# Performance work log

Measured on AMD Instinct MI355X. Metric: run time of the kernel, lower is better.

The kernel has to match this reference:

```python
import jax, jax.numpy as jnp
import numpy as np

B, T, D_MODEL = 1, 4096, 1024
H = 16
SEM_DIM, GEO_DIM, ATTN_DIM = 128, 256, 512
SEM_HD, GEO_HD, V_HD = SEM_DIM // H, GEO_DIM // H, ATTN_DIM // H
ROPE_BASE = 10000.0


def _split_heads(x, hd):
    # (B,T,H*hd) -> (B,H,T,hd)
    b, t, _ = x.shape
    return x.reshape(b, t, H, hd).transpose(0, 2, 1, 3)


def _rope(x, pos_offset, base=ROPE_BASE):
    # x: (B,H,T,rot) with rot == full geo head dim (rotate applies to first rot_dim;
    # here rot_dim == geo_head_dim so the whole vector rotates)
    rot = x.shape[-1]
    inv_freq = 1.0 / (base ** (jnp.arange(0, rot, 2, dtype=jnp.float32) / rot))
    t = jnp.arange(pos_offset, pos_offset + x.shape[2], dtype=jnp.float32)
    freqs = t[:, None] * inv_freq[None, :]            # (T, rot/2)
    cos = jnp.cos(freqs).astype(x.dtype)[None, None]  # (1,1,T,rot/2)
    sin = jnp.sin(freqs).astype(x.dtype)[None, None]
    x1, x2 = x[..., : rot // 2], x[..., rot // 2 :]
    return jnp.concatenate([x1 * cos - x2 * sin, x1 * sin + x2 * cos], axis=-1)


def setup_inputs() -> dict:
    key = jax.random.key(0)
    ks = jax.random.split(key, 8)
    s = lambda fan_in: 1.0 / np.sqrt(fan_in)
    inp = {
        "x": jax.random.normal(ks[0], (B, T, D_MODEL), dtype=jnp.float32),
        "q_sem_w": jax.random.uniform(ks[1], (SEM_DIM, D_MODEL), jnp.float32, -s(D_MODEL), s(D_MODEL)),
        "k_sem_w": jax.random.uniform(ks[2], (SEM_DIM, D_MODEL), jnp.float32, -s(D_MODEL), s(D_MODEL)),
        "q_geo_w": jax.random.uniform(ks[3], (GEO_DIM, D_MODEL), jnp.float32, -s(D_MODEL), s(D_MODEL)),
        "k_geo_w": jax.random.uniform(ks[4], (GEO_DIM, D_MODEL), jnp.float32, -s(D_MODEL), s(D_MODEL)),
        "v_w": jax.random.uniform(ks[5], (ATTN_DIM, D_MODEL), jnp.float32, -s(D_MODEL), s(D_MODEL)),
        "out_w": jax.random.uniform(ks[6], (D_MODEL, ATTN_DIM), jnp.float32, -s(ATTN_DIM), s(ATTN_DIM)),
        "logit_scale": jnp.zeros((H,), dtype=jnp.float32),
        "attn_mask": jnp.tril(jnp.ones((T, T), dtype=bool)),  # causal: True = attend
        "pos_offset": 0,
    }
    return inp


def reference(x, q_sem_w, k_sem_w, q_geo_w, k_geo_w, v_w, out_w, logit_scale, attn_mask, pos_offset):
    dt = x.dtype
    ninf = jnp.finfo(dt).min
    # decoupled projections
    qs = _split_heads(x @ q_sem_w.T, SEM_HD)   # (B,H,T,sem_hd)
    ksem = _split_heads(x @ k_sem_w.T, SEM_HD)
    qg = _split_heads(x @ q_geo_w.T, GEO_HD)   # (B,H,T,geo_hd)
    kg = _split_heads(x @ k_geo_w.T, GEO_HD)
    v = _split_heads(x @ v_w.T, V_HD)          # (B,H,T,v_hd)
    # RoPE on geometric stream only
    qg = _rope(qg, pos_offset)
    kg = _rope(kg, pos_offset)
    # combined scores, scaled as one concatenated QK dot product
    scale = 1.0 / np.sqrt(SEM_HD + GEO_HD)
    scores = (jnp.einsum("bhtd,bhsd->bhts", qs, ksem)
              + jnp.einsum("bhtd,bhsd->bhts", qg, kg)) * scale
    # learned per-head temperature
    scores = scores * jnp.exp(logit_scale)[None, :, None, None]
    scores = jnp.where(attn_mask[None, None], scores, ninf)
    attn = jax.nn.softmax(scores, axis=-1)
    out = jnp.einsum("bhts,bhsd->bhtd", attn, v)       # (B,H,T,v_hd)
    out = out.transpose(0, 2, 1, 3).reshape(B, T, ATTN_DIM)
    return out @ out_w.T                                # (B,T,d_model)
```

## Files before the change

### kernel.cpp

```cpp
#include <hip/hip_runtime.h>
#include <hip/hip_bf16.h>

typedef __attribute__((ext_vector_type(8))) short short8;
typedef __attribute__((ext_vector_type(4))) short short4v;
typedef __attribute__((ext_vector_type(4))) float f32x4;

#define TT 4096
#define DM 1024
#define NH 16
#define NPROJ 1280
#define DATTN 512

static __device__ __forceinline__ short f2bf(float f) {
  __hip_bfloat16 h = __float2bfloat16(f);
  return *reinterpret_cast<short*>(&h);
}

#define NB_X   (TT * DM / 4 / 256)
#define NB_OW  (DM * DATTN / 4 / 256)
#define NB_WC  (NPROJ * DM / 4 / 256)
__global__ __launch_bounds__(256) void k_prep(const float* __restrict__ x,
    const float* __restrict__ ow, const float* __restrict__ qs, const float* __restrict__ ks,
    const float* __restrict__ qg, const float* __restrict__ kg, const float* __restrict__ vw,
    __hip_bfloat16* __restrict__ Xbf, __hip_bfloat16* __restrict__ OW,
    __hip_bfloat16* __restrict__ Wcat) {
  const int b = blockIdx.x;
  if (b < NB_X) {
    const int i = b * 256 + threadIdx.x;
    float4 v = reinterpret_cast<const float4*>(x)[i];
    short4v o;
    o[0] = f2bf(v.x); o[1] = f2bf(v.y); o[2] = f2bf(v.z); o[3] = f2bf(v.w);
    reinterpret_cast<short4v*>(Xbf)[i] = o;
  } else if (b < NB_X + NB_OW) {
    const int i = (b - NB_X) * 256 + threadIdx.x;
    float4 v = reinterpret_cast<const float4*>(ow)[i];
    short4v o;
    o[0] = f2bf(v.x); o[1] = f2bf(v.y); o[2] = f2bf(v.z); o[3] = f2bf(v.w);
    reinterpret_cast<short4v*>(OW)[i] = o;
  } else {
    const int i = (b - NB_X - NB_OW) * 256 + threadIdx.x;
    const int idx = i * 4;
    const int row = idx >> 10;
    const int col = idx & 1023;
    const float* src;
    if (row < 128)      src = qs + (size_t)row * DM;
    else if (row < 256) src = ks + (size_t)(row - 128) * DM;
    else if (row < 512) src = qg + (size_t)(row - 256) * DM;
    else if (row < 768) src = kg + (size_t)(row - 512) * DM;
    else                src = vw + (size_t)(row - 768) * DM;
    float4 v = *reinterpret_cast<const float4*>(src + col);
    short4v o;
    o[0] = f2bf(v.x); o[1] = f2bf(v.y); o[2] = f2bf(v.z); o[3] = f2bf(v.w);
    *reinterpret_cast<short4v*>(Wcat + idx) = o;
  }
}

template<int EPI>
__global__ __launch_bounds__(256) void k_gemm_bt(const __hip_bfloat16* __restrict__ A,
    const __hip_bfloat16* __restrict__ B, void* __restrict__ Cv, int M, int N, int K,
    __hip_bfloat16* __restrict__ Qp, __hip_bfloat16* __restrict__ Kp,
    __hip_bfloat16* __restrict__ Vt, const float* __restrict__ ls,
    const int* __restrict__ posp) {
  __shared__ alignas(16) __hip_bfloat16 lA[2][2][64 * 32];
  __shared__ alignas(16) __hip_bfloat16 lB[2][2][128 * 32];
  const int tid = threadIdx.x;
  const int lane = tid & 63;
  const int wid = tid >> 6;
  const int m0 = blockIdx.x * 64, n0 = blockIdx.y * 128;
  const int wm = (wid >> 1) * 32, wn = (wid & 1) * 64;
  const int srow = tid >> 2;
  const int scol = (tid & 3) * 8;
  const int fr = lane & 15, fk = (lane >> 4) * 8;
  f32x4 acc[2][4];
  const f32x4 zz = {0.f, 0.f, 0.f, 0.f};
#pragma unroll
  for (int m = 0; m < 2; ++m)
#pragma unroll
    for (int n = 0; n < 4; ++n) acc[m][n] = zz;

  auto stage = [&](int kt, int buf) {
#pragma unroll
    for (int kk = 0; kk < 2; ++kk) {
      const int kcol = kt + kk * 32 + scol;
      const __hip_bfloat16* ga0 = A + (size_t)(m0 + srow) * K + kcol;
      const __hip_bfloat16* gb0 = B + (size_t)(n0 + srow) * K + kcol;
      const __hip_bfloat16* gb1 = B + (size_t)(n0 + 64 + srow) * K + kcol;
      __builtin_amdgcn_global_load_lds((const __attribute__((address_space(1))) void*)ga0,
          (__attribute__((address_space(3))) void*)(lA[buf][kk] + srow * 32 + scol), 16, 0, 0);
      __builtin_amdgcn_global_load_lds((const __attribute__((address_space(1))) void*)gb0,
          (__attribute__((address_space(3))) void*)(lB[buf][kk] + srow * 32 + scol), 16, 0, 0);
      __builtin_amdgcn_global_load_lds((const __attribute__((address_space(1))) void*)gb1,
          (__attribute__((address_space(3))) void*)(lB[buf][kk] + (64 + srow) * 32 + scol), 16, 0, 0);
    }
  };
  stage(0, 0);
  int buf = 0;
  for (int kt = 0; kt < K; kt += 64) {
    __syncthreads();
    if (kt + 64 < K) stage(kt + 64, buf ^ 1);
#pragma unroll
    for (int kk = 0; kk < 2; ++kk) {
      short8 af[2], bfr[4];
#pragma unroll
      for (int m = 0; m < 2; ++m)
        af[m] = *reinterpret_cast<const short8*>(lA[buf][kk] + (wm + m * 16 + fr) * 32 + fk);
#pragma unroll
      for (int n = 0; n < 4; ++n)
        bfr[n] = *reinterpret_cast<const short8*>(lB[buf][kk] + (wn + n * 16 + fr) * 32 + fk);
#pragma unroll
      for (int m = 0; m < 2; ++m)
#pragma unroll
        for (int n = 0; n < 4; ++n)
          acc[m][n] = __builtin_amdgcn_mfma_f32_16x16x32_bf16(af[m], bfr[n], acc[m][n], 0, 0, 0);
    }
    buf ^= 1;
  }
  const int cr = (lane >> 4) * 4, cc = lane & 15;
  if (EPI == 0) {
#pragma unroll
    for (int m = 0; m < 2; ++m)
#pragma unroll
      for (int n = 0; n < 4; ++n)
#pragma unroll
        for (int j = 0; j < 4; ++j) {
          const int row = m0 + wm + m * 16 + cr + j;
          const int col = n0 + wn + n * 16 + cc;
          ((float*)Cv)[(size_t)row * N + col] = acc[m][n][j];
        }
    return;
  }
  const int y = blockIdx.y;
  const float QSC = 0.20412414523193154f * 1.4426950408889634f;
  if (y < 2) {
    __hip_bfloat16* P = (y == 0) ? Qp : Kp;
    const __hip_bfloat16 zb = __float2bfloat16(0.f);
#pragma unroll
    for (int n = 0; n < 4; ++n) {
      const int cl = wn + n * 16 + cc;
      const int h = cl >> 3, d = cl & 7;
      const float sc = (y == 0) ? QSC * __expf(ls[h]) : 1.0f;
#pragma unroll
      for (int m = 0; m < 2; ++m)
#pragma unroll
        for (int j = 0; j < 4; ++j) {
          const int row = m0 + wm + m * 16 + cr + j;
          __hip_bfloat16* base = P + ((size_t)h * TT + row) * 32;
          base[d] = __float2bfloat16(acc[m][n][j] * sc);
          base[24 + d] = zb;
        }
    }
  } else if (y < 6) {
    const int isQ = (y < 4);
    __hip_bfloat16* P = isQ ? Qp : Kp;
    const int segbase = isQ ? 256 : 512;
    const float invf[8] = {1.0f, 0.31622776601683794f, 0.1f, 0.031622776601683794f,
                           0.01f, 0.0031622776601683794f, 0.001f, 0.00031622776601683794f};
    const float fr_ = invf[cc & 7];
    const float pofs = (float)posp[0];
    const int lo = (cc < 8);
    const int d = 8 + cc;
#pragma unroll
    for (int n = 0; n < 4; ++n) {
      const int h = (y * 128 + wn + n * 16 - segbase) >> 4;
      const float sc = isQ ? QSC * __expf(ls[h]) : 1.0f;
#pragma unroll
      for (int m = 0; m < 2; ++m)
#pragma unroll
        for (int j = 0; j < 4; ++j) {
          const int row = m0 + wm + m * 16 + cr + j;
          const float own = acc[m][n][j];
          const float oth = __shfl_xor(own, 8, 64);
          float ss, cs;
          __sincosf((row + pofs) * fr_, &ss, &cs);
          const float out = lo ? (own * cs - oth * ss) : (oth * ss + own * cs);
          P[((size_t)h * TT + row) * 32 + d] = __float2bfloat16(out * sc);
        }
    }
  } else {
#pragma unroll
    for (int n = 0; n < 4; ++n) {
      const int local = y * 128 + wn + n * 16 - 768 + cc;
      const int h = local >> 5, d = local & 31;
#pragma unroll
      for (int m = 0; m < 2; ++m) {
        short4v pk;
#pragma unroll
        for (int j = 0; j < 4; ++j) pk[j] = f2bf(acc[m][n][j]);
        const int row0 = m0 + wm + m * 16 + cr;
        *reinterpret_cast<short4v*>(Vt + ((size_t)h * 32 + d) * TT + row0) = pk;
      }
    }
  }
}

__global__ __launch_bounds__(256) void k_attn(const __hip_bfloat16* __restrict__ Qp,
    const __hip_bfloat16* __restrict__ Kp, const __hip_bfloat16* __restrict__ Vt,
    __hip_bfloat16* __restrict__ Ob) {
  __shared__ alignas(16) __hip_bfloat16 lK[2][64 * 32];
  __shared__ alignas(16) __hip_bfloat16 lV[2][32 * 64];
  __shared__ alignas(16) __hip_bfloat16 Plds[4][16][72];
  const int lin = blockIdx.x;
  const int xcd = lin & 7;
  const int idx = lin >> 3;
  const int h = xcd * 2 + (idx & 1);
  const int qb = 63 - (idx >> 1);
  const int nt = qb + 1;
  const int tid = threadIdx.x;
  const int lane = tid & 63, w = tid >> 6;
  const int g = lane >> 4, c = lane & 15;
  const int krow = (tid >> 6) * 16 + (tid & 15);
  const int kcol = ((tid >> 4) & 3) * 8;
  const int vrow = ((tid >> 6) & 1) * 16 + (tid & 15);
  const int vcol = ((tid >> 7) & 1) * 32 + ((tid >> 4) & 3) * 8;
  const __hip_bfloat16* Kh = Kp + (size_t)h * TT * 32 + (size_t)krow * 32 + kcol;
  const __hip_bfloat16* Vh = Vt + (size_t)h * 32 * TT + (size_t)vrow * TT + vcol;
  const f32x4 zz = {0.f, 0.f, 0.f, 0.f};

  const int qrow = qb * 64 + w * 16 + c;
  const short8 qf =
      *reinterpret_cast<const short8*>(Qp + ((size_t)h * TT + qrow) * 32 + 8 * g);
  f32x4 o0 = zz, o1 = zz;
  float mst = -1e30f, lsum = 0.f;
  int cur = 0;
  __builtin_amdgcn_global_load_lds(
      (const __attribute__((address_space(1))) void*)Kh,
      (__attribute__((address_space(3))) void*)(lK[0] + tid * 8), 16, 0, 0);
  __builtin_amdgcn_global_load_lds(
      (const __attribute__((address_space(1))) void*)Vh,
      (__attribute__((address_space(3))) void*)(lV[0] + tid * 8), 16, 0, 0);

  for (int it = 0; it < nt; ++it) {
    __syncthreads();
    if (it + 1 < nt) {
      const int kv1 = (it + 1) * 64;
      __builtin_amdgcn_global_load_lds(
          (const __attribute__((address_space(1))) void*)(Kh + (size_t)kv1 * 32),
          (__attribute__((address_space(3))) void*)(lK[cur ^ 1] + tid * 8), 16, 0, 0);
      __builtin_amdgcn_global_load_lds(
          (const __attribute__((address_space(1))) void*)(Vh + kv1),
          (__attribute__((address_space(3))) void*)(lV[cur ^ 1] + tid * 8), 16, 0, 0);
    }
    const char* kb = (const char*)lK[cur];
    short8 kf[4];
#pragma unroll
    for (int ct = 0; ct < 4; ++ct)
      kf[ct] = *reinterpret_cast<const short8*>(kb + ct * 1024 + lane * 16);
    const char* vb = (const char*)lV[cur];
    const short8 v00 = *reinterpret_cast<const short8*>(vb + lane * 16);
    const short8 v10 = *reinterpret_cast<const short8*>(vb + 1024 + lane * 16);
    const short8 v01 = *reinterpret_cast<const short8*>(vb + 2048 + lane * 16);
    const short8 v11 = *reinterpret_cast<const short8*>(vb + 3072 + lane * 16);
    f32x4 s[4];
#pragma unroll
    for (int ct = 0; ct < 4; ++ct)
      s[ct] = __builtin_amdgcn_mfma_f32_16x16x32_bf16(kf[ct], qf, zz, 0, 0, 0);
    if (it == nt - 1) {
#pragma unroll
      for (int ct = 0; ct < 4; ++ct)
#pragma unroll
        for (int j = 0; j < 4; ++j)
          if (ct * 16 + g * 4 + j > w * 16 + c) s[ct][j] = -1e30f;
    }
    float m01 = fmaxf(fmaxf(s[0][0], s[0][1]), fmaxf(s[0][2], s[0][3]));
    float m23 = fmaxf(fmaxf(s[1][0], s[1][1]), fmaxf(s[1][2], s[1][3]));
    float m45 = fmaxf(fmaxf(s[2][0], s[2][1]), fmaxf(s[2][2], s[2][3]));
    float m67 = fmaxf(fmaxf(s[3][0], s[3][1]), fmaxf(s[3][2], s[3][3]));
    float pm_ = fmaxf(fmaxf(m01, m23), fmaxf(m45, m67));
    if (__any(pm_ > mst + 8.0f)) {
      float pm2 = fmaxf(pm_, __shfl_xor(pm_, 16, 64));
      pm2 = fmaxf(pm2, __shfl_xor(pm2, 32, 64));
      const float nm = fmaxf(mst, pm2);
      const float alpha = exp2f(mst - nm);
      mst = nm;
      lsum *= alpha;
#pragma unroll
      for (int j = 0; j < 4; ++j) { o0[j] *= alpha; o1[j] *= alpha; }
    }
    float ts = 0.f;
#pragma unroll
    for (int ct = 0; ct < 4; ++ct) {
#pragma unroll
      for (int j = 0; j < 4; ++j) s[ct][j] = exp2f(s[ct][j] - mst);
      ts += (s[ct][0] + s[ct][1]) + (s[ct][2] + s[ct][3]);
    }
    lsum += ts;
#pragma unroll
    for (int ct = 0; ct < 4; ++ct) {
      float2 p01; p01.x = s[ct][0]; p01.y = s[ct][1];
      float2 p23; p23.x = s[ct][2]; p23.y = s[ct][3];
      __hip_bfloat162 b01 = __float22bfloat162_rn(p01);
      __hip_bfloat162 b23 = __float22bfloat162_rn(p23);
      *reinterpret_cast<__hip_bfloat162*>(&Plds[w][c][ct * 16 + g * 4]) = b01;
      *reinterpret_cast<__hip_bfloat162*>(&Plds[w][c][ct * 16 + g * 4 + 2]) = b23;
    }
    const short8 pf0 = *reinterpret_cast<const short8*>(&Plds[w][c][8 * g]);
    const short8 pf1 = *reinterpret_cast<const short8*>(&Plds[w][c][32 + 8 * g]);
    o0 = __builtin_amdgcn_mfma_f32_16x16x32_bf16(v00, pf0, o0, 0, 0, 0);
    o0 = __builtin_amdgcn_mfma_f32_16x16x32_bf16(v01, pf1, o0, 0, 0, 0);
    o1 = __builtin_amdgcn_mfma_f32_16x16x32_bf16(v10, pf0, o1, 0, 0, 0);
    o1 = __builtin_amdgcn_mfma_f32_16x16x32_bf16(v11, pf1, o1, 0, 0, 0);
    cur ^= 1;
  }
  lsum += __shfl_xor(lsum, 16, 64);
  lsum += __shfl_xor(lsum, 32, 64);
  const float inv = 1.0f / lsum;
  __hip_bfloat16* dst = Ob + (size_t)qrow * DATTN + h * 32;
  short4v w0, w1;
#pragma unroll
  for (int j = 0; j < 4; ++j) { w0[j] = f2bf(o0[j] * inv); w1[j] = f2bf(o1[j] * inv); }
  *reinterpret_cast<short4v*>(dst + g * 4) = w0;
  *reinterpret_cast<short4v*>(dst + 16 + g * 4) = w1;
}

extern "C" void kernel_launch(void* const* d_in, const int* in_sizes, int n_in,
                              void* d_out, int out_size, void* d_ws, size_t ws_size,
                              hipStream_t stream) {
  const float* x   = (const float*)d_in[0];
  const float* qsw = (const float*)d_in[1];
  const float* ksw = (const float*)d_in[2];
  const float* qgw = (const float*)d_in[3];
  const float* kgw = (const float*)d_in[4];
  const float* vw  = (const float*)d_in[5];
  const float* ow  = (const float*)d_in[6];
  const float* ls  = (const float*)d_in[7];
  const int* posp  = (const int*)d_in[9];

  size_t off = 0;
  auto alloc = [&](size_t bytes) {
    char* p = (char*)d_ws + off;
    off += (bytes + 255) & ~(size_t)255;
    return (void*)p;
  };
  __hip_bfloat16* Xbf  = (__hip_bfloat16*)alloc((size_t)TT * DM * 2);
  __hip_bfloat16* Wcat = (__hip_bfloat16*)alloc((size_t)NPROJ * DM * 2);
  __hip_bfloat16* OW   = (__hip_bfloat16*)alloc((size_t)DM * DATTN * 2);
  __hip_bfloat16* Qp   = (__hip_bfloat16*)alloc((size_t)NH * TT * 32 * 2);
  __hip_bfloat16* Kpk  = (__hip_bfloat16*)alloc((size_t)NH * TT * 32 * 2);
  __hip_bfloat16* Vt   = (__hip_bfloat16*)alloc((size_t)NH * 32 * TT * 2);
  __hip_bfloat16* Ob   = (__hip_bfloat16*)alloc((size_t)TT * DATTN * 2);

  k_prep<<<dim3(NB_X + NB_OW + NB_WC), 256, 0, stream>>>(x, ow, qsw, ksw, qgw, kgw, vw,
                                                         Xbf, OW, Wcat);
  k_gemm_bt<1><<<dim3(TT / 64, NPROJ / 128), 256, 0, stream>>>(Xbf, Wcat, nullptr,
      TT, NPROJ, DM, Qp, Kpk, Vt, ls, posp);
  k_attn<<<dim3(1024), 256, 0, stream>>>(Qp, Kpk, Vt, Ob);
  k_gemm_bt<0><<<dim3(TT / 64, DM / 128), 256, 0, stream>>>(Ob, OW, (void*)d_out,
      TT, DM, DATTN, nullptr, nullptr, nullptr, nullptr, nullptr);
}
```

Measured before the change: 112.5 us.

## Keep softmax P in registers and stage two KV tiles per barrier

Removes the per-wave LDS round trip for the probability matrix by packing P directly into MFMA B-operand registers. To match that register layout, the V operand is now gathered from LDS with permuted 8-byte reads instead of contiguous 16-byte reads. Each barrier round now stages two 64-row K/V tiles into a larger double buffer, which halves the number of __syncthreads calls. The cost is twice the LDS footprint per block, which may reduce occupancy, plus more scattered V reads.

```diff
diff --git a/kernel.cpp b/kernel.cpp
--- a/kernel.cpp
+++ b/kernel.cpp
@@ -14,6 +14,11 @@
 static __device__ __forceinline__ short f2bf(float f) {
   __hip_bfloat16 h = __float2bfloat16(f);
   return *reinterpret_cast<short*>(&h);
+}
+static __device__ __forceinline__ unsigned pk2(float a, float b) {
+  float2 t; t.x = a; t.y = b;
+  __hip_bfloat162 r = __float22bfloat162_rn(t);
+  return *reinterpret_cast<unsigned*>(&r);
 }
 
 #define NB_X   (TT * DM / 4 / 256)
@@ -196,15 +201,15 @@
 __global__ __launch_bounds__(256) void k_attn(const __hip_bfloat16* __restrict__ Qp,
     const __hip_bfloat16* __restrict__ Kp, const __hip_bfloat16* __restrict__ Vt,
     __hip_bfloat16* __restrict__ Ob) {
-  __shared__ alignas(16) __hip_bfloat16 lK[2][64 * 32];
-  __shared__ alignas(16) __hip_bfloat16 lV[2][32 * 64];
-  __shared__ alignas(16) __hip_bfloat16 Plds[4][16][72];
+  __shared__ alignas(16) __hip_bfloat16 lK[2][128 * 32];
+  __shared__ alignas(16) __hip_bfloat16 lV[2][32 * 128];
   const int lin = blockIdx.x;
   const int xcd = lin & 7;
   const int idx = lin >> 3;
   const int h = xcd * 2 + (idx & 1);
   const int qb = 63 - (idx >> 1);
   const int nt = qb + 1;
+  const int rounds = (nt + 1) >> 1;
   const int tid = threadIdx.x;
   const int lane = tid & 63, w = tid >> 6;
   const int g = lane >> 4, c = lane & 15;
@@ -215,90 +220,99 @@
   const __hip_bfloat16* Kh = Kp + (size_t)h * TT * 32 + (size_t)krow * 32 + kcol;
   const __hip_bfloat16* Vh = Vt + (size_t)h * 32 * TT + (size_t)vrow * TT + vcol;
   const f32x4 zz = {0.f, 0.f, 0.f, 0.f};
+  const int vb0 = (g >> 1) * 256 + c * 16 + 8 * (g & 1);
 
   const int qrow = qb * 64 + w * 16 + c;
   const short8 qf =
       *reinterpret_cast<const short8*>(Qp + ((size_t)h * TT + qrow) * 32 + 8 * g);
   f32x4 o0 = zz, o1 = zz;
   float mst = -1e30f, lsum = 0.f;
+
+  auto stage = [&](int r, int buf) {
+#pragma unroll
+    for (int sub = 0; sub < 2; ++sub) {
+      const int kv = r * 128 + sub * 64;
+      __builtin_amdgcn_global_load_lds(
+          (const __attribute__((address_space(1))) void*)(Kh + (size_t)kv * 32),
+          (__attribute__((address_space(3))) void*)(lK[buf] + sub * 2048 + tid * 8), 16, 0, 0);
+      __builtin_amdgcn_global_load_lds(
+          (const __attribute__((address_space(1))) void*)(Vh + kv),
+          (__attribute__((address_space(3))) void*)(lV[buf] + sub * 2048 + tid * 8), 16, 0, 0);
+    }
+  };
+  stage(0, 0);
   int cur = 0;
-  __builtin_amdgcn_global_load_lds(
-      (const __attribute__((address_space(1))) void*)Kh,
-      (__attribute__((address_space(3))) void*)(lK[0] + tid * 8), 16, 0, 0);
-  __builtin_amdgcn_global_load_lds(
-      (const __attribute__((address_space(1))) void*)Vh,
-      (__attribute__((address_space(3))) void*)(lV[0] + tid * 8), 16, 0, 0);
-
-  for (int it = 0; it < nt; ++it) {
+  for (int r = 0; r < rounds; ++r) {
     __syncthreads();
-    if (it + 1 < nt) {
-      const int kv1 = (it + 1) * 64;
-      __builtin_amdgcn_global_load_lds(
-          (const __attribute__((address_space(1))) void*)(Kh + (size_t)kv1 * 32),
-          (__attribute__((address_space(3))) void*)(lK[cur ^ 1] + tid * 8), 16, 0, 0);
-      __builtin_amdgcn_global_load_lds(
-          (const __attribute__((address_space(1))) void*)(Vh + kv1),
-          (__attribute__((address_space(3))) void*)(lV[cur ^ 1] + tid * 8), 16, 0, 0);
-    }
-    const char* kb = (const char*)lK[cur];
-    short8 kf[4];
-#pragma unroll
-    for (int ct = 0; ct < 4; ++ct)
-      kf[ct] = *reinterpret_cast<const short8*>(kb + ct * 1024 + lane * 16);
-    const char* vb = (const char*)lV[cur];
-    const short8 v00 = *reinterpret_cast<const short8*>(vb + lane * 16);
-    const short8 v10 = *reinterpret_cast<const short8*>(vb + 1024 + lane * 16);
-    const short8 v01 = *reinterpret_cast<const short8*>(vb + 2048 + lane * 16);
-    const short8 v11 = *reinterpret_cast<const short8*>(vb + 3072 + lane * 16);
-    f32x4 s[4];
-#pragma unroll
-    for (int ct = 0; ct < 4; ++ct)
-      s[ct] = __builtin_amdgcn_mfma_f32_16x16x32_bf16(kf[ct], qf, zz, 0, 0, 0);
-    if (it == nt - 1) {
+    if (r + 1 < rounds) stage(r + 1, cur ^ 1);
+#pragma unroll 2
+    for (int sub = 0; sub < 2; ++sub) {
+      const int it = 2 * r + sub;
+      if (it >= nt) break;
+      const char* kb = (const char*)lK[cur] + sub * 4096;
+      const char* vb = (const char*)lV[cur] + sub * 4096;
+      short8 kf[4];
 #pragma unroll
       for (int ct = 0; ct < 4; ++ct)
-#pragma unroll
-        for (int j = 0; j < 4; ++j)
-          if (ct * 16 + g * 4 + j > w * 16 + c) s[ct][j] = -1e30f;
-    }
-    float m01 = fmaxf(fmaxf(s[0][0], s[0][1]), fmaxf(s[0][2], s[0][3]));
-    float m23 = fmaxf(fmaxf(s[1][0], s[1][1]), fmaxf(s[1][2], s[1][3]));
-    float m45 = fmaxf(fmaxf(s[2][0], s[2][1]), fmaxf(s[2][2], s[2][3]));
-    float m67 = fmaxf(fmaxf(s[3][0], s[3][1]), fmaxf(s[3][2], s[3][3]));
-    float pm_ = fmaxf(fmaxf(m01, m23), fmaxf(m45, m67));
-    if (__any(pm_ > mst + 8.0f)) {
-      float pm2 = fmaxf(pm_, __shfl_xor(pm_, 16, 64));
-      pm2 = fmaxf(pm2, __shfl_xor(pm2, 32, 64));
-      const float nm = fmaxf(mst, pm2);
-      const float alpha = exp2f(mst - nm);
-      mst = nm;
-      lsum *= alpha;
-#pragma unroll
-      for (int j = 0; j < 4; ++j) { o0[j] *= alpha; o1[j] *= alpha; }
-    }
-    float ts = 0.f;
-#pragma unroll
-    for (int ct = 0; ct < 4; ++ct) {
-#pragma unroll
-      for (int j = 0; j < 4; ++j) s[ct][j] = exp2f(s[ct][j] - mst);
-      ts += (s[ct][0] + s[ct][1]) + (s[ct][2] + s[ct][3]);
-    }
-    lsum += ts;
-#pragma unroll
-    for (int ct = 0; ct < 4; ++ct) {
-      float2 p01; p01.x = s[ct][0]; p01.y = s[ct][1];
-      float2 p23; p23.x = s[ct][2]; p23.y = s[ct][3];
-      __hip_bfloat162 b01 = __float22bfloat162_rn(p01);
-      __hip_bfloat162 b23 = __float22bfloat162_rn(p23);
-      *reinterpret_cast<__hip_bfloat162*>(&Plds[w][c][ct * 16 + g * 4]) = b01;
-      *reinterpret_cast<__hip_bfloat162*>(&Plds[w][c][ct * 16 + g * 4 + 2]) = b23;
-    }
-    const short8 pf0 = *reinterpret_cast<const short8*>(&Plds[w][c][8 * g]);
-    const short8 pf1 = *reinterpret_cast<const short8*>(&Plds[w][c][32 + 8 * g]);
-    o0 = __builtin_amdgcn_mfma_f32_16x16x32_bf16(v00, pf0, o0, 0, 0, 0);
-    o0 = __builtin_amdgcn_mfma_f32_16x16x32_bf16(v01, pf1, o0, 0, 0, 0);
-    o1 = __builtin_amdgcn_mfma_f32_16x16x32_bf16(v10, pf0, o1, 0, 0, 0);
-    o1 = __builtin_amdgcn_mfma_f32_16x16x32_bf16(v11, pf1, o1, 0, 0, 0);
+        kf[ct] = *reinterpret_cast<const short8*>(kb + ct * 1024 + lane * 16);
+      union U8 { unsigned u[4]; short8 v8; };
+      U8 aA0, aA1, aB0, aB1;
+      *reinterpret_cast<uint2*>(&aA0.u[0]) = *reinterpret_cast<const uint2*>(vb + vb0);
+      *reinterpret_cast<uint2*>(&aA0.u[2]) = *reinterpret_cast<const uint2*>(vb + vb0 + 512);
+      *reinterpret_cast<uint2*>(&aB0.u[0]) = *reinterpret_cast<const uint2*>(vb + vb0 + 1024);
+      *reinterpret_cast<uint2*>(&aB0.u[2]) = *reinterpret_cast<const uint2*>(vb + vb0 + 1536);
+      *reinterpret_cast<uint2*>(&aA1.u[0]) = *reinterpret_cast<const uint2*>(vb + vb0 + 2048);
+      *reinterpret_cast<uint2*>(&aA1.u[2]) = *reinterpret_cast<const uint2*>(vb + vb0 + 2560);
+      *reinterpret_cast<uint2*>(&aB1.u[0]) = *reinterpret_cast<const uint2*>(vb + vb0 + 3072);
+      *reinterpret_cast<uint2*>(&aB1.u[2]) = *reinterpret_cast<const uint2*>(vb + vb0 + 3584);
+      f32x4 s[4];
+#pragma unroll
+      for (int ct = 0; ct < 4; ++ct)
+        s[ct] = __builtin_amdgcn_mfma_f32_16x16x32_bf16(kf[ct], qf, zz, 0, 0, 0);
+      if (it == nt - 1) {
+#pragma unroll
+        for (int ct = 0; ct < 4; ++ct)
+#pragma unroll
+          for (int j = 0; j < 4; ++j)
+            if (ct * 16 + g * 4 + j > w * 16 + c) s[ct][j] = -1e30f;
+      }
+      float m01 = fmaxf(fmaxf(s[0][0], s[0][1]), fmaxf(s[0][2], s[0][3]));
+      float m23 = fmaxf(fmaxf(s[1][0], s[1][1]), fmaxf(s[1][2], s[1][3]));
+      float m45 = fmaxf(fmaxf(s[2][0], s[2][1]), fmaxf(s[2][2], s[2][3]));
+      float m67 = fmaxf(fmaxf(s[3][0], s[3][1]), fmaxf(s[3][2], s[3][3]));
+      float pm_ = fmaxf(fmaxf(m01, m23), fmaxf(m45, m67));
+      if (__any(pm_ > mst + 8.0f)) {
+        float pm2 = fmaxf(pm_, __shfl_xor(pm_, 16, 64));
+        pm2 = fmaxf(pm2, __shfl_xor(pm2, 32, 64));
+        const float nm = fmaxf(mst, pm2);
+        const float alpha = exp2f(mst - nm);
+        mst = nm;
+        lsum *= alpha;
+#pragma unroll
+        for (int j = 0; j < 4; ++j) { o0[j] *= alpha; o1[j] *= alpha; }
+      }
+      float ts = 0.f;
+#pragma unroll
+      for (int ct = 0; ct < 4; ++ct) {
+#pragma unroll
+        for (int j = 0; j < 4; ++j) s[ct][j] = exp2f(s[ct][j] - mst);
+        ts += (s[ct][0] + s[ct][1]) + (s[ct][2] + s[ct][3]);
+      }
+      lsum += ts;
+      U8 pb0, pb1;
+      pb0.u[0] = pk2(s[0][0], s[0][1]);
+      pb0.u[1] = pk2(s[0][2], s[0][3]);
+      pb0.u[2] = pk2(s[1][0], s[1][1]);
+      pb0.u[3] = pk2(s[1][2], s[1][3]);
+      pb1.u[0] = pk2(s[2][0], s[2][1]);
+      pb1.u[1] = pk2(s[2][2], s[2][3]);
+      pb1.u[2] = pk2(s[3][0], s[3][1]);
+      pb1.u[3] = pk2(s[3][2], s[3][3]);
+      o0 = __builtin_amdgcn_mfma_f32_16x16x32_bf16(aA0.v8, pb0.v8, o0, 0, 0, 0);
+      o0 = __builtin_amdgcn_mfma_f32_16x16x32_bf16(aA1.v8, pb1.v8, o0, 0, 0, 0);
+      o1 = __builtin_amdgcn_mfma_f32_16x16x32_bf16(aB0.v8, pb0.v8, o1, 0, 0, 0);
+      o1 = __builtin_amdgcn_mfma_f32_16x16x32_bf16(aB1.v8, pb1.v8, o1, 0, 0, 0);
+    }
     cur ^= 1;
   }
   lsum += __shfl_xor(lsum, 16, 64);
```

After: 113.5 us. Within noise of the previous version (+0.9%).
